# Kernel optimization log

Hardware: AMD Instinct MI355X
Metric: run time of the kernel (lower is better)

## Reference

```python
import jax, jax.numpy as jnp
import numpy as np

N_NODES = 50000


def _gcn_conv(h, src, dst, W, b, n_nodes):
    """PyG GCNConv: add self-loops, symmetric deg^{-1/2} normalization,
    linear transform, scatter-add aggregation at target nodes."""
    h = h @ W  # [N, out]
    # self-loops
    loop = jnp.arange(n_nodes, dtype=src.dtype)
    s = jnp.concatenate([src, loop])  # source j
    d = jnp.concatenate([dst, loop])  # target i
    ones = jnp.ones(s.shape[0], dtype=h.dtype)
    deg = jax.ops.segment_sum(ones, d, num_segments=n_nodes)  # in-degree incl. self-loop
    dinv = jnp.where(deg > 0, jax.lax.rsqrt(deg), 0.0)
    norm = dinv[s] * dinv[d]  # [E+N]
    msg = h[s] * norm[:, None]  # gather + scale, [E+N, out]
    out = jax.ops.segment_sum(msg, d, num_segments=n_nodes)  # scatter-add
    return out + b


def reference(x, edge_index, q_emb, W1, b1, W2, b2, Wq, bq):
    src, dst = edge_index[0], edge_index[1]
    n = x.shape[0]
    # dropout rates are 0.0 -> identity
    h1 = jax.nn.relu(_gcn_conv(x, src, dst, W1, b1, n))
    h2 = _gcn_conv(h1, src, dst, W2, b2, n)
    ques = q_emb @ Wq + bq
    return (ques, h2)


def setup_inputs() -> dict:
    key = jax.random.key(0)
    ks = jax.random.split(key, 9)
    d = 128
    sc = 1.0 / np.sqrt(d)
    return {
        "x": jax.random.normal(ks[0], (N_NODES, d), dtype=jnp.float32),
        "edge_index": jax.random.randint(ks[1], (2, 800000), 0, N_NODES, dtype=jnp.int64),
        "q_emb": jax.random.normal(ks[2], (20000, d), dtype=jnp.float32),
        "W1": jax.random.normal(ks[3], (d, d), dtype=jnp.float32) * sc,
        "b1": jax.random.normal(ks[4], (d,), dtype=jnp.float32) * 0.01,
        "W2": jax.random.normal(ks[5], (d, d), dtype=jnp.float32) * sc,
        "b2": jax.random.normal(ks[6], (d,), dtype=jnp.float32) * 0.01,
        "Wq": jax.random.normal(ks[7], (d, d), dtype=jnp.float32) * sc,
        "bq": jax.random.normal(ks[8], (d,), dtype=jnp.float32) * 0.01,
    }
```

## Files before the change

### kernel.cpp

```cpp
#include <hip/hip_runtime.h>

#define D 128
#define NS 8
#define NFB 1024
#define CAP 64

typedef __attribute__((ext_vector_type(8))) short bf16x8;
typedef __attribute__((ext_vector_type(4))) float f32x4;

__device__ __forceinline__ unsigned short f2b(float v) {
    unsigned u = __float_as_uint(v);
    unsigned r = u + 0x7fffu + ((u >> 16) & 1u);
    return (unsigned short)(r >> 16);
}
__device__ __forceinline__ float b2f(unsigned short h) {
    return __uint_as_float(((unsigned)h) << 16);
}


__global__ __launch_bounds__(256) void prep(int* __restrict__ cnt, int N, int nbz,
                                            const float* __restrict__ W1,
                                            const float* __restrict__ W2,
                                            const float* __restrict__ Wq,
                                            unsigned short* __restrict__ o1,
                                            unsigned short* __restrict__ o2,
                                            unsigned short* __restrict__ oq) {
    int b = blockIdx.x;
    if (b < nbz) {
        int idx = b * 256 + threadIdx.x;
        if (idx * 4 + 4 <= N) {
            ((int4*)cnt)[idx] = make_int4(0, 0, 0, 0);
        } else {
            for (int k = idx * 4; k < N; ++k) cnt[k] = 0;
        }
        return;
    }
    int t = (b - nbz) * 256 + threadIdx.x;
    int which = t >> 14;
    int r = t & 16383;
    int n = r >> 7, k = r & 127;
    const float* W = (which == 0) ? W1 : (which == 1) ? W2 : Wq;
    unsigned short* o = (which == 0) ? o1 : (which == 1) ? o2 : oq;
    o[r] = f2b(W[k * D + n]);
}


__device__ __forceinline__ void gemm_body(const float* Af,
                                          const unsigned short* __restrict__ Wth,
                                          const float* bias, unsigned short* Cb,
                                          float* Cf, int M, int bid, int outf,
                                          char* smem) {
    int lane = threadIdx.x & 63;
    int wave = threadIdx.x >> 6;
    int m16 = (bid * 4 + wave) * 16;
    if (m16 >= M) return;
    int mrow = lane & 15;
    int quad = lane >> 4;

    f32x4 acc[8];
#pragma unroll
    for (int nt = 0; nt < 8; ++nt) acc[nt] = (f32x4){0.f, 0.f, 0.f, 0.f};

    int arow = m16 + mrow;

#pragma unroll
    for (int ks = 0; ks < 4; ++ks) {
        bf16x8 ah, al;
        const float* ap = Af + (size_t)arow * D + ks * 32 + quad * 8;
        float4 v0 = *(const float4*)ap;
        float4 v1 = *(const float4*)(ap + 4);
        float vv[8] = {v0.x, v0.y, v0.z, v0.w, v1.x, v1.y, v1.z, v1.w};
#pragma unroll
        for (int j = 0; j < 8; ++j) {
            unsigned short h = f2b(vv[j]);
            ah[j] = (short)h;
            al[j] = (short)f2b(vv[j] - b2f(h));
        }
#pragma unroll
        for (int nt = 0; nt < 8; ++nt) {
            bf16x8 wf = *(const bf16x8*)(Wth + (size_t)(nt * 16 + mrow) * D + ks * 32 + quad * 8);
            acc[nt] = __builtin_amdgcn_mfma_f32_16x16x32_bf16(ah, wf, acc[nt], 0, 0, 0);
            acc[nt] = __builtin_amdgcn_mfma_f32_16x16x32_bf16(al, wf, acc[nt], 0, 0, 0);
        }
    }

    if (outf == 0) {
        unsigned short* myl = (unsigned short*)smem + wave * 16 * 136;
#pragma unroll
        for (int nt = 0; nt < 8; ++nt) {
            int col = nt * 16 + mrow;
#pragma unroll
            for (int r = 0; r < 4; ++r)
                myl[(quad * 4 + r) * 136 + col] = f2b(acc[nt][r]);
        }
#pragma unroll
        for (int R = 0; R < 16; ++R) {
            unsigned int v = *(const unsigned int*)&myl[R * 136 + lane * 2];
            ((unsigned int*)(Cb + (size_t)(m16 + R) * D))[lane] = v;
        }
    } else {
#pragma unroll
        for (int nt = 0; nt < 8; ++nt) {
            int col = nt * 16 + mrow;
            float bv = bias[col];
#pragma unroll
            for (int r = 0; r < 4; ++r)
                Cf[(size_t)(m16 + quad * 4 + r) * D + col] = acc[nt][r] + bv;
        }
    }
}

__global__ __launch_bounds__(256) void frontfill(const float* __restrict__ x,
                                                 const float* __restrict__ q,
                                                 const unsigned short* __restrict__ Wth1,
                                                 const unsigned short* __restrict__ Wthq,
                                                 const float* __restrict__ bq,
                                                 unsigned short* __restrict__ Cb,
                                                 float* __restrict__ outq,
                                                 const int* __restrict__ src,
                                                 const int* __restrict__ dst,
                                                 int* __restrict__ cnt,
                                                 int* __restrict__ colv,
                                                 int N, int MQ, int E, int nbN, int nps) {
    __shared__ char smem[4 * 16 * 136 * 2];
    int b = blockIdx.x;
    if (b < NFB) {
        int s = b & (NS - 1);
        int chunk = b >> 3;
        int nchunks = NFB >> 3;
        int lo = s * nps, hi = lo + nps;
        if (hi > N) hi = N;
        int stride = nchunks * 256;
        for (int e = chunk * 256 + threadIdx.x; e < E; e += stride) {
            int d = dst[e];
            if (d >= lo && d < hi) {
                int slot = atomicAdd(&cnt[d], 1);
                if (slot < CAP) colv[(size_t)d * CAP + slot] = src[e];
            }
        }
        return;
    }
    b -= NFB;
    if (b < nbN)
        gemm_body(x, Wth1, nullptr, Cb, nullptr, N, b, 0, smem);
    else
        gemm_body(q, Wthq, bq, nullptr, outq, MQ, b - nbN, 1, smem);
}

__device__ __forceinline__ void agg_node(const bf16x8* __restrict__ T8,
                                         const int* __restrict__ colv,
                                         const int* __restrict__ cnt,
                                         int i, int lane, int g, int l16,
                                         float acc[8]) {
#pragma unroll
    for (int k = 0; k < 8; ++k) acc[k] = 0.f;
    int deg = cnt[i];
    int ci = (deg < CAP) ? deg : CAP;
    int e0 = i * CAP;
    int e1 = e0 + ci;
    for (int base = e0; base < e1; base += 64) {
        int cb = e1 - base;
        if (cb > 64) cb = 64;
        int jv = 0;
        float wv = 0.f;
        if (lane < cb) {
            jv = colv[base + lane];
            wv = rsqrtf((float)(cnt[jv] + 1));
        }
        int t = 0;
        for (; t + 16 <= cb; t += 16) {
            int j0 = __shfl(jv, t + g);
            int j1 = __shfl(jv, t + 4 + g);
            int j2 = __shfl(jv, t + 8 + g);
            int j3 = __shfl(jv, t + 12 + g);
            float w0 = __shfl(wv, t + g);
            float w1 = __shfl(wv, t + 4 + g);
            float w2 = __shfl(wv, t + 8 + g);
            float w3 = __shfl(wv, t + 12 + g);
            bf16x8 r0 = T8[(size_t)j0 * 16 + l16];
            bf16x8 r1 = T8[(size_t)j1 * 16 + l16];
            bf16x8 r2 = T8[(size_t)j2 * 16 + l16];
            bf16x8 r3 = T8[(size_t)j3 * 16 + l16];
#pragma unroll
            for (int k = 0; k < 8; ++k) acc[k] = fmaf(w0, b2f((unsigned short)r0[k]), acc[k]);
#pragma unroll
            for (int k = 0; k < 8; ++k) acc[k] = fmaf(w1, b2f((unsigned short)r1[k]), acc[k]);
#pragma unroll
            for (int k = 0; k < 8; ++k) acc[k] = fmaf(w2, b2f((unsigned short)r2[k]), acc[k]);
#pragma unroll
            for (int k = 0; k < 8; ++k) acc[k] = fmaf(w3, b2f((unsigned short)r3[k]), acc[k]);
        }
        for (; t < cb; t += 4) {
            int j = __shfl(jv, t + g);
            float w = __shfl(wv, t + g);
            if (w > 0.f) {
                bf16x8 r = T8[(size_t)j * 16 + l16];
#pragma unroll
                for (int k = 0; k < 8; ++k) acc[k] = fmaf(w, b2f((unsigned short)r[k]), acc[k]);
            }
        }
    }
#pragma unroll
    for (int k = 0; k < 8; ++k) {
        acc[k] += __shfl_xor(acc[k], 16);
        acc[k] += __shfl_xor(acc[k], 32);
    }
}

__global__ __launch_bounds__(512) void agg1_gemm(const unsigned short* __restrict__ Tb,
                                                 const int* __restrict__ colv,
                                                 const int* __restrict__ cnt,
                                                 const float* __restrict__ bias,
                                                 const unsigned short* __restrict__ Wth2,
                                                 unsigned short* __restrict__ Cb2,
                                                 int N) {
    __shared__ unsigned short AH[16 * 136];
    __shared__ unsigned short AL[16 * 136];
    int wave = threadIdx.x >> 6;
    int lane = threadIdx.x & 63;
    int g = lane >> 4;
    int l16 = lane & 15;
    int node0 = blockIdx.x * 16;
    const bf16x8* T8 = (const bf16x8*)Tb;

#pragma unroll
    for (int sub = 0; sub < 2; ++sub) {
        int row = wave * 2 + sub;
        int i = node0 + row;
        float acc[8];
        if (i < N) {
            agg_node(T8, colv, cnt, i, lane, g, l16, acc);
            if (g == 0) {
                int deg = cnt[i];
                float di = rsqrtf((float)(deg + 1));
                bf16x8 selfr = T8[(size_t)i * 16 + l16];
                float4 b0 = ((const float4*)bias)[l16 * 2];
                float4 b1v = ((const float4*)bias)[l16 * 2 + 1];
                float bb[8] = {b0.x, b0.y, b0.z, b0.w, b1v.x, b1v.y, b1v.z, b1v.w};
                bf16x8 h, l;
#pragma unroll
                for (int k = 0; k < 8; ++k) {
                    float r = di * acc[k] + di * di * b2f((unsigned short)selfr[k]) + bb[k];
                    r = fmaxf(r, 0.f);
                    unsigned short hh = f2b(r);
                    h[k] = (short)hh;
                    l[k] = (short)f2b(r - b2f(hh));
                }
                *(bf16x8*)&AH[row * 136 + l16 * 8] = h;
                *(bf16x8*)&AL[row * 136 + l16 * 8] = l;
            }
        } else if (g == 0) {
            bf16x8 z = (bf16x8){0, 0, 0, 0, 0, 0, 0, 0};
            *(bf16x8*)&AH[row * 136 + l16 * 8] = z;
            *(bf16x8*)&AL[row * 136 + l16 * 8] = z;
        }
    }
    __syncthreads();

    int nt = wave;
    int mrow = l16;
    int quad = g;
    f32x4 acc2 = (f32x4){0.f, 0.f, 0.f, 0.f};
#pragma unroll
    for (int ks = 0; ks < 4; ++ks) {
        bf16x8 ah = *(const bf16x8*)&AH[mrow * 136 + ks * 32 + quad * 8];
        bf16x8 al = *(const bf16x8*)&AL[mrow * 136 + ks * 32 + quad * 8];
        bf16x8 wf = *(const bf16x8*)(Wth2 + (size_t)(nt * 16 + mrow) * D + ks * 32 + quad * 8);
        acc2 = __builtin_amdgcn_mfma_f32_16x16x32_bf16(ah, wf, acc2, 0, 0, 0);
        acc2 = __builtin_amdgcn_mfma_f32_16x16x32_bf16(al, wf, acc2, 0, 0, 0);
    }
    __syncthreads();
    {
        int col = nt * 16 + mrow;
#pragma unroll
        for (int r = 0; r < 4; ++r)
            AH[(quad * 4 + r) * 136 + col] = f2b(acc2[r]);
    }
    __syncthreads();
#pragma unroll
    for (int k = 0; k < 2; ++k) {
        int idx = threadIdx.x + k * 512;
        int row = idx >> 6;
        int c = idx & 63;
        if (node0 + row < N) {
            unsigned int v = *(const unsigned int*)&AH[row * 136 + c * 2];
            ((unsigned int*)(Cb2 + (size_t)(node0 + row) * D))[c] = v;
        }
    }
}

__global__ __launch_bounds__(512) void aggregate2(const unsigned short* __restrict__ Tb,
                                                  const int* __restrict__ colv,
                                                  const int* __restrict__ cnt,
                                                  const float* __restrict__ bias,
                                                  float* __restrict__ Of, int N) {
    int wave = threadIdx.x >> 6;
    int lane = threadIdx.x & 63;
    int i = blockIdx.x * 8 + wave;
    if (i >= N) return;
    int g = lane >> 4;
    int l16 = lane & 15;
    const bf16x8* T8 = (const bf16x8*)Tb;

    float acc[8];
    agg_node(T8, colv, cnt, i, lane, g, l16, acc);

    if (g == 0) {
        int deg = cnt[i];
        float di = rsqrtf((float)(deg + 1));
        bf16x8 selfr = T8[(size_t)i * 16 + l16];
        float4 b0 = ((const float4*)bias)[l16 * 2];
        float4 b1v = ((const float4*)bias)[l16 * 2 + 1];
        float bb[8] = {b0.x, b0.y, b0.z, b0.w, b1v.x, b1v.y, b1v.z, b1v.w};
        float4 r0, r1;
        r0.x = di * acc[0] + di * di * b2f((unsigned short)selfr[0]) + bb[0];
        r0.y = di * acc[1] + di * di * b2f((unsigned short)selfr[1]) + bb[1];
        r0.z = di * acc[2] + di * di * b2f((unsigned short)selfr[2]) + bb[2];
        r0.w = di * acc[3] + di * di * b2f((unsigned short)selfr[3]) + bb[3];
        r1.x = di * acc[4] + di * di * b2f((unsigned short)selfr[4]) + bb[4];
        r1.y = di * acc[5] + di * di * b2f((unsigned short)selfr[5]) + bb[5];
        r1.z = di * acc[6] + di * di * b2f((unsigned short)selfr[6]) + bb[6];
        r1.w = di * acc[7] + di * di * b2f((unsigned short)selfr[7]) + bb[7];
        ((float4*)Of)[(size_t)i * 32 + l16 * 2] = r0;
        ((float4*)Of)[(size_t)i * 32 + l16 * 2 + 1] = r1;
    }
}


static inline char* carve(char*& w, size_t bytes) {
    char* p = w;
    w += (bytes + 255) & ~(size_t)255;
    return p;
}

extern "C" void kernel_launch(void* const* d_in, const int* in_sizes, int n_in,
                              void* d_out, int out_size, void* d_ws, size_t ws_size,
                              hipStream_t stream) {
    const float* x  = (const float*)d_in[0];
    const int*   ei = (const int*)d_in[1];
    const float* q  = (const float*)d_in[2];
    const float* W1 = (const float*)d_in[3];
    const float* b1 = (const float*)d_in[4];
    const float* W2 = (const float*)d_in[5];
    const float* b2 = (const float*)d_in[6];
    const float* Wq = (const float*)d_in[7];
    const float* bq = (const float*)d_in[8];

    int N  = in_sizes[0] / D;
    int E  = in_sizes[1] / 2;
    int MQ = in_sizes[2] / D;

    const int* srcv = ei;
    const int* dstv = ei + E;

    char* w = (char*)d_ws;
    unsigned short* Cb   = (unsigned short*)carve(w, (size_t)N * D * 2);
    unsigned short* Cb2  = (unsigned short*)carve(w, (size_t)N * D * 2);
    int*            colv = (int*)carve(w, (size_t)N * CAP * 4);
    int*            cnt  = (int*)carve(w, (size_t)N * 4);
    unsigned short* Wth1 = (unsigned short*)carve(w, D * D * 2);
    unsigned short* Wth2 = (unsigned short*)carve(w, D * D * 2);
    unsigned short* Wthq = (unsigned short*)carve(w, D * D * 2);

    float* outq = (float*)d_out;
    float* outh = outq + (size_t)MQ * D;

    int nbz = (N / 4 + 255) / 256;
    int nps = (N + NS - 1) / NS;
    int nbN = (N + 63) / 64;
    int nbQ = (MQ + 63) / 64;

    prep<<<nbz + 192, 256, 0, stream>>>(cnt, N, nbz, W1, W2, Wq, Wth1, Wth2, Wthq);
    frontfill<<<NFB + nbN + nbQ, 256, 0, stream>>>(x, q, Wth1, Wthq, bq, Cb, outq,
                                                   srcv, dstv, cnt, colv,
                                                   N, MQ, E, nbN, nps);
    agg1_gemm<<<(N + 15) / 16, 512, 0, stream>>>(Cb, colv, cnt, b1, Wth2, Cb2, N);
    aggregate2<<<(N + 7) / 8, 512, 0, stream>>>(Cb2, colv, cnt, b2, outh, N);
}
```

Baseline: 246.8 us.

## Vectorize edge bucketing, prescale layer-2 features by dinv, unweighted second aggregation

The edge-bucketing phase drops its 8-way destination-range partitioning and instead reads src/dst as int4 vectors, doing the atomic slot insertion for every edge in one pass over fewer blocks. The first-layer GEMM epilogue now multiplies each output row by its own deg^{-1/2} before storing, so the second aggregation can sum neighbor rows without per-edge normalization. It uses an inlined four-way unrolled gather loop and applies only the target's dinv once at the end. The aim is to remove the repeated edge scans of the partitioned fill and the per-edge scaling work, at the cost of more contended atomics per block and slightly different bf16 rounding.

```diff
diff --git a/kernel.cpp b/kernel.cpp
--- a/kernel.cpp
+++ b/kernel.cpp
@@ -1,8 +1,7 @@
 #include <hip/hip_runtime.h>
 
 #define D 128
-#define NS 8
-#define NFB 1024
+#define NFB 256
 #define CAP 64
 
 typedef __attribute__((ext_vector_type(8))) short bf16x8;
@@ -121,22 +120,31 @@
                                                  const int* __restrict__ dst,
                                                  int* __restrict__ cnt,
                                                  int* __restrict__ colv,
-                                                 int N, int MQ, int E, int nbN, int nps) {
+                                                 int N, int MQ, int E, int nbN) {
     __shared__ char smem[4 * 16 * 136 * 2];
     int b = blockIdx.x;
     if (b < NFB) {
-        int s = b & (NS - 1);
-        int chunk = b >> 3;
-        int nchunks = NFB >> 3;
-        int lo = s * nps, hi = lo + nps;
-        if (hi > N) hi = N;
-        int stride = nchunks * 256;
-        for (int e = chunk * 256 + threadIdx.x; e < E; e += stride) {
+        const int4* d4 = (const int4*)dst;
+        const int4* s4 = (const int4*)src;
+        int n4 = E >> 2;
+        int stride = NFB * 256;
+        for (int idx = b * 256 + threadIdx.x; idx < n4; idx += stride) {
+            int4 dv = d4[idx];
+            int4 sv = s4[idx];
+            int slot;
+            slot = atomicAdd(&cnt[dv.x], 1);
+            if (slot < CAP) colv[(size_t)dv.x * CAP + slot] = sv.x;
+            slot = atomicAdd(&cnt[dv.y], 1);
+            if (slot < CAP) colv[(size_t)dv.y * CAP + slot] = sv.y;
+            slot = atomicAdd(&cnt[dv.z], 1);
+            if (slot < CAP) colv[(size_t)dv.z * CAP + slot] = sv.z;
+            slot = atomicAdd(&cnt[dv.w], 1);
+            if (slot < CAP) colv[(size_t)dv.w * CAP + slot] = sv.w;
+        }
+        for (int e = (n4 << 2) + b * 256 + threadIdx.x; e < E; e += stride) {
             int d = dst[e];
-            if (d >= lo && d < hi) {
-                int slot = atomicAdd(&cnt[d], 1);
-                if (slot < CAP) colv[(size_t)d * CAP + slot] = src[e];
-            }
+            int slot = atomicAdd(&cnt[d], 1);
+            if (slot < CAP) colv[(size_t)d * CAP + slot] = src[e];
         }
         return;
     }
@@ -273,8 +281,11 @@
     {
         int col = nt * 16 + mrow;
 #pragma unroll
-        for (int r = 0; r < 4; ++r)
-            AH[(quad * 4 + r) * 136 + col] = f2b(acc2[r]);
+        for (int r = 0; r < 4; ++r) {
+            int gi = node0 + quad * 4 + r;
+            float dr = (gi < N) ? rsqrtf((float)(cnt[gi] + 1)) : 0.f;
+            AH[(quad * 4 + r) * 136 + col] = f2b(acc2[r] * dr);
+        }
     }
     __syncthreads();
 #pragma unroll
@@ -303,24 +314,63 @@
     const bf16x8* T8 = (const bf16x8*)Tb;
 
     float acc[8];
-    agg_node(T8, colv, cnt, i, lane, g, l16, acc);
+#pragma unroll
+    for (int k = 0; k < 8; ++k) acc[k] = 0.f;
+
+    int deg = cnt[i];
+    int ci = (deg < CAP) ? deg : CAP;
+    int e0 = i * CAP;
+    int e1 = e0 + ci;
+    for (int base = e0; base < e1; base += 64) {
+        int cb = e1 - base;
+        if (cb > 64) cb = 64;
+        int jv = (lane < cb) ? colv[base + lane] : 0;
+        int t = 0;
+        for (; t + 16 <= cb; t += 16) {
+            int j0 = __shfl(jv, t + g);
+            int j1 = __shfl(jv, t + 4 + g);
+            int j2 = __shfl(jv, t + 8 + g);
+            int j3 = __shfl(jv, t + 12 + g);
+            bf16x8 r0 = T8[(size_t)j0 * 16 + l16];
+            bf16x8 r1 = T8[(size_t)j1 * 16 + l16];
+            bf16x8 r2 = T8[(size_t)j2 * 16 + l16];
+            bf16x8 r3 = T8[(size_t)j3 * 16 + l16];
+#pragma unroll
+            for (int k = 0; k < 8; ++k)
+                acc[k] += b2f((unsigned short)r0[k]) + b2f((unsigned short)r1[k]) +
+                          b2f((unsigned short)r2[k]) + b2f((unsigned short)r3[k]);
+        }
+        for (; t < cb; t += 4) {
+            int j = __shfl(jv, t + g);
+            if (t + g < cb) {
+                bf16x8 r = T8[(size_t)j * 16 + l16];
+#pragma unroll
+                for (int k = 0; k < 8; ++k) acc[k] += b2f((unsigned short)r[k]);
+            }
+        }
+    }
+
+#pragma unroll
+    for (int k = 0; k < 8; ++k) {
+        acc[k] += __shfl_xor(acc[k], 16);
+        acc[k] += __shfl_xor(acc[k], 32);
+    }
 
     if (g == 0) {
-        int deg = cnt[i];
         float di = rsqrtf((float)(deg + 1));
         bf16x8 selfr = T8[(size_t)i * 16 + l16];
         float4 b0 = ((const float4*)bias)[l16 * 2];
         float4 b1v = ((const float4*)bias)[l16 * 2 + 1];
         float bb[8] = {b0.x, b0.y, b0.z, b0.w, b1v.x, b1v.y, b1v.z, b1v.w};
         float4 r0, r1;
-        r0.x = di * acc[0] + di * di * b2f((unsigned short)selfr[0]) + bb[0];
-        r0.y = di * acc[1] + di * di * b2f((unsigned short)selfr[1]) + bb[1];
-        r0.z = di * acc[2] + di * di * b2f((unsigned short)selfr[2]) + bb[2];
-        r0.w = di * acc[3] + di * di * b2f((unsigned short)selfr[3]) + bb[3];
-        r1.x = di * acc[4] + di * di * b2f((unsigned short)selfr[4]) + bb[4];
-        r1.y = di * acc[5] + di * di * b2f((unsigned short)selfr[5]) + bb[5];
-        r1.z = di * acc[6] + di * di * b2f((unsigned short)selfr[6]) + bb[6];
-        r1.w = di * acc[7] + di * di * b2f((unsigned short)selfr[7]) + bb[7];
+        r0.x = di * (acc[0] + b2f((unsigned short)selfr[0])) + bb[0];
+        r0.y = di * (acc[1] + b2f((unsigned short)selfr[1])) + bb[1];
+        r0.z = di * (acc[2] + b2f((unsigned short)selfr[2])) + bb[2];
+        r0.w = di * (acc[3] + b2f((unsigned short)selfr[3])) + bb[3];
+        r1.x = di * (acc[4] + b2f((unsigned short)selfr[4])) + bb[4];
+        r1.y = di * (acc[5] + b2f((unsigned short)selfr[5])) + bb[5];
+        r1.z = di * (acc[6] + b2f((unsigned short)selfr[6])) + bb[6];
+        r1.w = di * (acc[7] + b2f((unsigned short)selfr[7])) + bb[7];
         ((float4*)Of)[(size_t)i * 32 + l16 * 2] = r0;
         ((float4*)Of)[(size_t)i * 32 + l16 * 2 + 1] = r1;
     }
@@ -366,14 +416,13 @@
     float* outh = outq + (size_t)MQ * D;
 
     int nbz = (N / 4 + 255) / 256;
-    int nps = (N + NS - 1) / NS;
     int nbN = (N + 63) / 64;
     int nbQ = (MQ + 63) / 64;
 
     prep<<<nbz + 192, 256, 0, stream>>>(cnt, N, nbz, W1, W2, Wq, Wth1, Wth2, Wthq);
     frontfill<<<NFB + nbN + nbQ, 256, 0, stream>>>(x, q, Wth1, Wthq, bq, Cb, outq,
                                                    srcv, dstv, cnt, colv,
-                                                   N, MQ, E, nbN, nps);
+                                                   N, MQ, E, nbN);
     agg1_gemm<<<(N + 15) / 16, 512, 0, stream>>>(Cb, colv, cnt, b1, Wth2, Cb2, N);
     aggregate2<<<(N + 7) / 8, 512, 0, stream>>>(Cb2, colv, cnt, b2, outh, N);
 }
```

Result: faster. 236.6 us (-4.1%).
